# Kernel tuning notes

Hardware: AMD Instinct MI355X
Metric: run time of the kernel (lower is better)

## Reference

```python
import jax, jax.numpy as jnp
import numpy as np
from functools import partial

B, N, C = 16, 10647, 80   # batch, total anchors (YOLOv3@416), num classes
K = 2048                  # max candidates kept per image before NMS
SCORE_THR = 0.5
IOU_THR = 0.5


def setup_inputs() -> dict:
    key = jax.random.key(0)
    # [B, N, 4+1+C]: xywh (normalized), objectness, class probs
    y_pred = jax.random.uniform(key, (B, N, 5 + C), dtype=jnp.float32)
    return {"y_pred": y_pred}


def _xywh_to_corners(b):
    x, y, w, h = b[..., 0], b[..., 1], b[..., 2], b[..., 3]
    return jnp.stack([x - w / 2, y - h / 2, x + w / 2, y + h / 2], axis=-1)


def _pairwise_iou(boxes):  # boxes [K,4] corners -> [K,K]
    x1, y1, x2, y2 = boxes[:, 0], boxes[:, 1], boxes[:, 2], boxes[:, 3]
    area = jnp.maximum(x2 - x1, 0.0) * jnp.maximum(y2 - y1, 0.0)
    ix1 = jnp.maximum(x1[:, None], x1[None, :])
    iy1 = jnp.maximum(y1[:, None], y1[None, :])
    ix2 = jnp.minimum(x2[:, None], x2[None, :])
    iy2 = jnp.minimum(y2[:, None], y2[None, :])
    inter = jnp.maximum(ix2 - ix1, 0.0) * jnp.maximum(iy2 - iy1, 0.0)
    union = area[:, None] + area[None, :] - inter
    return inter / jnp.maximum(union, 1e-9)


def _greedy_nms_keep(boxes, valid):  # boxes [K,4] sorted by score desc, valid [K] bool
    iou = _pairwise_iou(boxes)
    idxs = jnp.arange(K)

    def body(i, keep):
        suppress = keep[i] & (idxs > i) & (iou[i] > IOU_THR)
        return keep & ~suppress

    return jax.lax.fori_loop(0, K, body, valid)


def reference(y_pred):
    boxes_xywh = y_pred[..., :4]           # [B,N,4]
    obj = y_pred[..., 4]                   # [B,N]
    cls_probs = y_pred[..., 5:]            # [B,N,C]
    scores = obj * jnp.max(cls_probs, axis=-1)  # [B,N]

    # top-K candidates per image (sorted by score desc)
    scores_k, idx = jax.lax.top_k(scores, K)             # [B,K]
    boxes_k = jnp.take_along_axis(boxes_xywh, idx[:, :, None], axis=1)  # [B,K,4]
    corners = _xywh_to_corners(boxes_k)                  # [B,K,4]

    valid = scores_k > SCORE_THR                          # [B,K]
    # NMS keep mask is a non-differentiable selection
    keep = jax.vmap(_greedy_nms_keep)(
        jax.lax.stop_gradient(corners), valid)            # [B,K] bool
    keep_f = keep.astype(scores_k.dtype)

    out_boxes = corners * keep_f[:, :, None]
    out_scores = scores_k * keep_f
    return jnp.concatenate([out_boxes, out_scores[:, :, None]], axis=-1)  # [B,K,5]
```

## Files before the change

kernel.cpp:

```cpp
#include <hip/hip_runtime.h>

#define BATCH 16
#define NROW  10647
#define ROWF  85
#define NCLS  80
#define KTOP  2048
#define MPAD  16384
#define SCORE_THR 0.5f
#define IOU_THR   0.5f

typedef unsigned long long u64;
typedef unsigned int u32;

__device__ __forceinline__ u32 enc_f32(float f) {
    u32 u = __float_as_uint(f);
    return (u & 0x80000000u) ? ~u : (u | 0x80000000u);
}
__device__ __forceinline__ float dec_f32(u32 e) {
    u32 u = (e & 0x80000000u) ? (e & 0x7FFFFFFFu) : ~e;
    return __uint_as_float(u);
}
__device__ __forceinline__ float bcast(float v, int ii) {
    return __uint_as_float(__builtin_amdgcn_readlane(__float_as_uint(v), ii));
}
__device__ __forceinline__ u64 rl64(u64 v, int l) {
    u32 lo = __builtin_amdgcn_readlane((u32)(v & 0xFFFFFFFFull), l);
    u32 hi = __builtin_amdgcn_readlane((u32)(v >> 32), l);
    return ((u64)hi << 32) | (u64)lo;
}
__device__ __forceinline__ void gload_lds16(const void* g, void* lds) {
    __builtin_amdgcn_global_load_lds(
        (const __attribute__((address_space(1))) void*)g,
        (__attribute__((address_space(3))) void*)lds, 16, 0, 0);
}
__device__ __forceinline__ void bar_lds() {
    asm volatile("s_waitcnt lgkmcnt(0)" ::: "memory");
    __builtin_amdgcn_s_barrier();
    __builtin_amdgcn_sched_barrier(0);
}

template<int J>
__device__ __forceinline__ void reg_pass(u64 v[8], int tid, int k) {
    #pragma unroll
    for (int r = 0; r < 8; ++r) {
        if (!(r & J)) {
            bool desc = (((tid * 8 + r) & k) == 0);
            u64 a = v[r], b = v[r | J];
            u64 mx = a > b ? a : b, mn = a > b ? b : a;
            v[r]     = desc ? mx : mn;
            v[r | J] = desc ? mn : mx;
        }
    }
}

__device__ __forceinline__ void shfl_pass(u64 v[8], int tid, int k, int d) {
    const bool upper = (tid & d) == 0;
    const bool desc = (((tid * 8) & k) == 0);
    const bool keepmax = (desc == upper);
    #pragma unroll
    for (int r = 0; r < 8; ++r) {
        u64 pv = __shfl_xor(v[r], d);
        u64 mx = v[r] > pv ? v[r] : pv, mn = v[r] > pv ? pv : v[r];
        v[r] = keepmax ? mx : mn;
    }
}

__device__ __forceinline__ void lds_pass(u64 v[8], int tid, u64* sm, int k, int d) {
    __syncthreads();
    #pragma unroll
    for (int r = 0; r < 8; ++r) sm[r * 256 + tid] = v[r];
    __syncthreads();
    const bool upper = (tid & d) == 0;
    const bool desc = (((tid * 8) & k) == 0);
    const bool keepmax = (desc == upper);
    const int pt = tid ^ d;
    #pragma unroll
    for (int r = 0; r < 8; ++r) {
        u64 pv = sm[r * 256 + pt];
        u64 mx = v[r] > pv ? v[r] : pv, mn = v[r] > pv ? pv : v[r];
        v[r] = keepmax ? mx : mn;
    }
}

__device__ __forceinline__ void sort2048_desc(u64 v[8], int tid, u64* sm) {
    reg_pass<1>(v, tid, 2);
    reg_pass<2>(v, tid, 4); reg_pass<1>(v, tid, 4);
    for (int k = 8; k <= 2048; k <<= 1) {
        for (int j = k >> 1; j >= 8; j >>= 1) {
            int d = j >> 3;
            if (d <= 32) shfl_pass(v, tid, k, d);
            else         lds_pass(v, tid, sm, k, d);
        }
        reg_pass<4>(v, tid, k); reg_pass<2>(v, tid, k); reg_pass<1>(v, tid, k);
    }
}

__device__ __forceinline__ void cleanup2048_desc(u64 v[8], int tid, u64* sm) {
    lds_pass(v, tid, sm, 4096, 128);
    lds_pass(v, tid, sm, 4096, 64);
    for (int d = 32; d >= 1; d >>= 1) shfl_pass(v, tid, 4096, d);
    reg_pass<4>(v, tid, 4096); reg_pass<2>(v, tid, 4096); reg_pass<1>(v, tid, 4096);
}

__global__ void score_kernel(const float* __restrict__ yp, u64* __restrict__ keys) {
    __shared__ float tile[128 * ROWF];
    const int tileIdx = blockIdx.x;
    const int b = blockIdx.y;
    const int tid = threadIdx.x;
    const int batch_lim = NROW * ROWF;
    const int tile_base = tileIdx * 128 * ROWF;

    if (tile_base < batch_lim) {
        const float* src = yp + (long long)b * batch_lim + tile_base;
        int lim_e = batch_lim - tile_base;
        if (lim_e > 128 * ROWF) lim_e = 128 * ROWF;
        const int head = (4 - ((3 * b) & 3)) & 3;
        if (lim_e >= 8) {
            const int nv = (lim_e - head) >> 2;
            for (int e = tid; e < head; e += 256) tile[e] = src[e];
            const float4* s4 = (const float4*)(src + head);
            for (int q = tid; q < nv; q += 256) {
                float4 v = s4[q];
                int o = head + q * 4;
                tile[o] = v.x; tile[o + 1] = v.y; tile[o + 2] = v.z; tile[o + 3] = v.w;
            }
            for (int e = head + nv * 4 + tid; e < lim_e; e += 256) tile[e] = src[e];
        } else {
            for (int e = tid; e < lim_e; e += 256) tile[e] = src[e];
        }
    }
    __syncthreads();

    {
        const int row = tid >> 1;
        const int half = tid & 1;
        int gr = tileIdx * 128 + row;
        const float* r = &tile[row * ROWF];
        float m = r[5 + half * 40];
        #pragma unroll
        for (int c = 1; c < 40; ++c) m = fmaxf(m, r[5 + half * 40 + c]);
        float mo = __uint_as_float(__shfl_xor(__float_as_uint(m), 1));
        if (half == 0 && gr < NROW) {
            float s = r[4] * fmaxf(m, mo);
            keys[(long long)b * MPAD + gr] =
                ((u64)enc_f32(s) << 32) | (u64)(0xFFFFFFFFu - (u32)gr);
        } else if (half == 0) {
            keys[(long long)b * MPAD + gr] = 0ULL;
        }
    }
}

__global__ void chunk_sort_kernel(u64* __restrict__ keys) {
    __shared__ u64 sm[2048];
    const int b = blockIdx.y, c = blockIdx.x, tid = threadIdx.x;
    u64* base = keys + (long long)b * MPAD + c * 2048;
    u64 v[8];
    #pragma unroll
    for (int r = 0; r < 8; ++r) v[r] = base[tid * 8 + r];
    sort2048_desc(v, tid, sm);
    #pragma unroll
    for (int r = 0; r < 8; ++r) base[tid * 8 + r] = v[r];
}

__global__ void merge_r1_kernel(const u64* __restrict__ keysA, u64* __restrict__ keysB) {
    __shared__ u64 sm[2048];
    const int b = blockIdx.y, c = blockIdx.x, tid = threadIdx.x;
    const u64* a = keysA + (long long)b * MPAD + c * 4096;
    u64 v[8];
    #pragma unroll
    for (int r = 0; r < 8; ++r) {
        int e = tid * 8 + r;
        u64 va = a[e], vb = a[4095 - e];
        v[r] = va > vb ? va : vb;
    }
    cleanup2048_desc(v, tid, sm);
    u64* d = keysB + (long long)b * MPAD + c * 2048;
    #pragma unroll
    for (int r = 0; r < 8; ++r) d[tid * 8 + r] = v[r];
}

__global__ void merge_r23_gather_kernel(const u64* __restrict__ keysB,
                                        const float* __restrict__ yp,
                                        float* __restrict__ sx1, float* __restrict__ sy1,
                                        float* __restrict__ sx2, float* __restrict__ sy2,
                                        float* __restrict__ sar, float* __restrict__ ssc) {
    __shared__ u64 sm[2048];
    const int b = blockIdx.x, tid = threadIdx.x;
    const u64* a = keysB + (long long)b * MPAD;
    u64 v[8];
    #pragma unroll
    for (int r = 0; r < 8; ++r) {
        int e = tid * 8 + r;
        u64 va = a[e], vb = a[2048 + 2047 - e];
        v[r] = va > vb ? va : vb;
    }
    cleanup2048_desc(v, tid, sm);
    #pragma unroll
    for (int r = 0; r < 8; ++r) {
        int e = tid * 8 + r;
        u64 vb = a[4096 + 2047 - e];
        v[r] = v[r] > vb ? v[r] : vb;
    }
    cleanup2048_desc(v, tid, sm);

    #pragma unroll
    for (int r = 0; r < 8; ++r) {
        u64 key = v[r];
        float s = dec_f32((u32)(key >> 32));
        u32 idx = 0xFFFFFFFFu - (u32)(key & 0xFFFFFFFFu);
        const float* rp = yp + (long long)b * NROW * ROWF + (long long)idx * ROWF;
        float x = rp[0], y = rp[1], w = rp[2], h = rp[3];
        float hx = w * 0.5f, hy = h * 0.5f;
        float a1 = x - hx, b1 = y - hy, a2 = x + hx, b2 = y + hy;
        int o = b * KTOP + tid * 8 + r;
        sx1[o] = a1; sy1[o] = b1; sx2[o] = a2; sy2[o] = b2;
        sar[o] = fmaxf(a2 - a1, 0.f) * fmaxf(b2 - b1, 0.f);
        ssc[o] = s;
    }
}

__global__ void mask_kernel(const float* __restrict__ sx1, const float* __restrict__ sy1,
                            const float* __restrict__ sx2, const float* __restrict__ sy2,
                            const float* __restrict__ sar, u64* __restrict__ mask,
                            u64* __restrict__ diag) {
    const int b = blockIdx.y;
    const int t = blockIdx.x * 4 + (threadIdx.x >> 6);
    const int lane = threadIdx.x & 63;

    int rb = (int)((65.0f - sqrtf(4225.0f - 8.0f * (float)t)) * 0.5f);
    while (rb * (65 - rb) / 2 > t) --rb;
    while ((rb + 1) * (64 - rb) / 2 <= t) ++rb;
    const int cb = rb + t - rb * (65 - rb) / 2;

    const int oi = b * KTOP + rb * 64 + lane;
    const int oj = b * KTOP + cb * 64 + lane;
    const float rx1 = sx1[oi], ry1 = sy1[oi], rx2 = sx2[oi], ry2 = sy2[oi], ra = sar[oi];
    const float cx1 = sx1[oj], cy1 = sy1[oj], cx2 = sx2[oj], cy2 = sy2[oj], ca = sar[oj];
    const bool dg = (rb == cb);

    u64 myword = 0ULL;
    for (int ii = 0; ii < 64; ++ii) {
        float ax1 = bcast(rx1, ii), ay1 = bcast(ry1, ii);
        float ax2 = bcast(rx2, ii), ay2 = bcast(ry2, ii);
        float aa  = bcast(ra,  ii);
        float ix1 = fmaxf(ax1, cx1);
        float iy1 = fmaxf(ay1, cy1);
        float ix2 = fminf(ax2, cx2);
        float iy2 = fminf(ay2, cy2);
        float inter = fmaxf(ix2 - ix1, 0.f) * fmaxf(iy2 - iy1, 0.f);
        float uni = aa + ca - inter;
        float iou = inter / fmaxf(uni, 1e-9f);
        bool cond = (iou > IOU_THR) && (!dg || (lane > ii));
        u64 bal = __ballot(cond);
        if (lane == ii) myword = bal;
    }
    mask[(long long)(b * KTOP + rb * 64 + lane) * 32 + cb] = myword;
    if (dg) diag[(long long)b * 2048 + rb * 64 + lane] = myword;
}

__global__ void nms_out_kernel(const float* __restrict__ sx1, const float* __restrict__ sy1,
                               const float* __restrict__ sx2, const float* __restrict__ sy2,
                               const float* __restrict__ ssc,
                               const u64* __restrict__ mask,
                               const u64* __restrict__ diag, float* __restrict__ out) {
    __shared__ u64 slots[4][2048];
    __shared__ u64 pend[8][32];
    __shared__ u64 curs;
    __shared__ u64 sbits64[32];
    __shared__ u64 keepw[32];
    const int b = blockIdx.x;
    const int tid = threadIdx.x;
    const int lane = tid & 63;
    const int wave = tid >> 6;
    const u64* mb = mask + (long long)(b * KTOP) * 32;
    const char* mbc = (const char*)mb;
    const u64* dg = diag + (long long)b * 2048;

    auto issue_block = [&](int B) {
        const char* src = mbc + (size_t)B * 16384;
        char* dst = (char*)&slots[B & 3][0];
        #pragma unroll
        for (int i = 0; i < 16; ++i)
            gload_lds16(src + i * 1024 + lane * 16, dst + i * 1024);
    };

    {
        const float* sp = ssc + b * KTOP + tid * 8;
        float4 sa = *(const float4*)(sp);
        float4 sb = *(const float4*)(sp + 4);
        unsigned bits =
            (unsigned)(sa.x > SCORE_THR)       | ((unsigned)(sa.y > SCORE_THR) << 1) |
            ((unsigned)(sa.z > SCORE_THR) << 2) | ((unsigned)(sa.w > SCORE_THR) << 3) |
            ((unsigned)(sb.x > SCORE_THR) << 4) | ((unsigned)(sb.y > SCORE_THR) << 5) |
            ((unsigned)(sb.z > SCORE_THR) << 6) | ((unsigned)(sb.w > SCORE_THR) << 7);
        ((unsigned char*)sbits64)[tid] = (unsigned char)bits;
    }
    u64 dia = 0ULL;
    if (wave == 0) dia = dg[lane];
    if (wave >= 1) issue_block(wave - 1);
    __syncthreads();

    u64 myw = 0ULL;
    if (wave == 0 && lane < 32) myw = sbits64[lane];

    #pragma unroll 1
    for (int w = 0; w < 32; ++w) {
        const u64* blk = &slots[w & 3][0];

        if (wave == 0) {
            u64 dia_next = 0ULL;
            if (w < 31) dia_next = dg[(w + 1) * 64 + lane];
            u64 cur = rl64(myw, w);
            #pragma unroll
            for (int p = 0; p < 4; ++p) {
                u64 dd[16];
                #pragma unroll
                for (int i = 0; i < 16; ++i) dd[i] = rl64(dia, p * 16 + i);
                #pragma unroll
                for (int i = 0; i < 16; ++i) {
                    u64 m = ((cur >> (p * 16 + i)) & 1ULL) ? dd[i] : 0ULL;
                    cur &= ~m;
                }
            }
            if (lane == 0) curs = cur;
            dia = dia_next;
        } else {
            const int rr = wave - 1;
            if ((w % 3) == rr && w + 3 < 32) issue_block(w + 3);
            if (((w + 1) % 3) == rr)
                asm volatile("s_waitcnt vmcnt(0)" ::: "memory");
        }
        bar_lds();

        {
            u64 curv = curs;
            const int col = tid & 31;
            const int rg  = tid >> 5;
            const u64* rp = blk + (size_t)rg * 256 + col;
            u32 bits8 = (u32)(curv >> (rg * 8)) & 0xFFu;
            u64 acc = 0ULL;
            #pragma unroll
            for (int i = 0; i < 8; ++i) {
                u64 t = rp[(size_t)i * 32];
                acc |= ((bits8 >> i) & 1u) ? t : 0ULL;
            }
            pend[rg][col] = acc;
        }
        bar_lds();

        if (wave == 0 && lane < 32) {
            u64 cur = curs;
            u64 s = ((pend[0][lane] | pend[1][lane]) | (pend[2][lane] | pend[3][lane]))
                  | ((pend[4][lane] | pend[5][lane]) | (pend[6][lane] | pend[7][lane]));
            if (lane == w) myw = cur;
            else if (lane > w) myw &= ~s;
        }
    }

    if (wave == 0 && lane < 32) keepw[lane] = myw;
    __syncthreads();

    for (int t = tid; t < KTOP; t += 256) {
        int o = b * KTOP + t;
        float f = ((keepw[t >> 6] >> (t & 63)) & 1ULL) ? 1.0f : 0.0f;
        float* op = out + (long long)o * 5;
        op[0] = sx1[o] * f;
        op[1] = sy1[o] * f;
        op[2] = sx2[o] * f;
        op[3] = sy2[o] * f;
        op[4] = ssc[o] * f;
    }
}

extern "C" void kernel_launch(void* const* d_in, const int* in_sizes, int n_in,
                              void* d_out, int out_size, void* d_ws, size_t ws_size,
                              hipStream_t stream) {
    const float* yp = (const float*)d_in[0];
    float* out = (float*)d_out;
    char* ws = (char*)d_ws;

    const size_t KEYS_BYTES = (size_t)BATCH * MPAD * sizeof(u64);
    const size_t MASK_BYTES = (size_t)BATCH * KTOP * 32 * sizeof(u64);
    const size_t SOA_BYTES  = (size_t)6 * BATCH * KTOP * sizeof(float);
    u64* keysA = (u64*)ws;
    u64* keysB = (u64*)(ws + KEYS_BYTES);
    u64* mask  = (u64*)ws;
    float* soa = (float*)(ws + MASK_BYTES);
    u64* diag  = (u64*)(ws + MASK_BYTES + SOA_BYTES);
    const int SA = BATCH * KTOP;
    float* sx1 = soa + 0 * SA;
    float* sy1 = soa + 1 * SA;
    float* sx2 = soa + 2 * SA;
    float* sy2 = soa + 3 * SA;
    float* sar = soa + 4 * SA;
    float* ssc = soa + 5 * SA;

    score_kernel<<<dim3(96, BATCH), 256, 0, stream>>>(yp, keysA);
    chunk_sort_kernel<<<dim3(6, BATCH), 256, 0, stream>>>(keysA);
    merge_r1_kernel<<<dim3(3, BATCH), 256, 0, stream>>>(keysA, keysB);
    merge_r23_gather_kernel<<<BATCH, 256, 0, stream>>>(keysB, yp,
                                                       sx1, sy1, sx2, sy2, sar, ssc);
    mask_kernel<<<dim3(132, BATCH), 256, 0, stream>>>(sx1, sy1, sx2, sy2, sar,
                                                      mask, diag);
    nms_out_kernel<<<BATCH, 256, 0, stream>>>(sx1, sy1, sx2, sy2, ssc,
                                              mask, diag, out);
}
```

Measured before the change: 161.8 us.

## Pack NMS suppression mask as upper-triangular rows to halve mask traffic

The mask kernel now writes only the upper-triangular column blocks of each 64-row block into a packed per-image layout, with row stride padded to an even word count. The NMS kernel streams only those words into LDS per row block, so the serial NMS stage loads about half as much mask data. In exchange, addressing becomes variable-stride and the per-block load loop is no longer fully unrolled. Columns left of the diagonal are clamped to a valid offset and rely on existing masking to ignore them.

```diff
diff --git a/kernel.cpp b/kernel.cpp
--- a/kernel.cpp
+++ b/kernel.cpp
@@ -8,6 +8,7 @@
 #define MPAD  16384
 #define SCORE_THR 0.5f
 #define IOU_THR   0.5f
+#define PKWORDS 34816
 
 typedef unsigned long long u64;
 typedef unsigned int u32;
@@ -28,6 +29,8 @@
     u32 hi = __builtin_amdgcn_readlane((u32)(v >> 32), l);
     return ((u64)hi << 32) | (u64)lo;
 }
+__device__ __forceinline__ int wpad(int B) { return 32 - B + (B & 1); }
+__device__ __forceinline__ int soff(int B) { return 32 * B - (B * (B - 1)) / 2 + (B >> 1); }
 __device__ __forceinline__ void gload_lds16(const void* g, void* lds) {
     __builtin_amdgcn_global_load_lds(
         (const __attribute__((address_space(1))) void*)g,
@@ -221,7 +224,7 @@
 
 __global__ void mask_kernel(const float* __restrict__ sx1, const float* __restrict__ sy1,
                             const float* __restrict__ sx2, const float* __restrict__ sy2,
-                            const float* __restrict__ sar, u64* __restrict__ mask,
+                            const float* __restrict__ sar, u64* __restrict__ packed,
                             u64* __restrict__ diag) {
     const int b = blockIdx.y;
     const int t = blockIdx.x * 4 + (threadIdx.x >> 6);
@@ -254,14 +257,15 @@
         u64 bal = __ballot(cond);
         if (lane == ii) myword = bal;
     }
-    mask[(long long)(b * KTOP + rb * 64 + lane) * 32 + cb] = myword;
+    const int wB = wpad(rb);
+    packed[(long long)b * PKWORDS + 64 * soff(rb) + lane * wB + (cb - rb)] = myword;
     if (dg) diag[(long long)b * 2048 + rb * 64 + lane] = myword;
 }
 
 __global__ void nms_out_kernel(const float* __restrict__ sx1, const float* __restrict__ sy1,
                                const float* __restrict__ sx2, const float* __restrict__ sy2,
                                const float* __restrict__ ssc,
-                               const u64* __restrict__ mask,
+                               const u64* __restrict__ packed,
                                const u64* __restrict__ diag, float* __restrict__ out) {
     __shared__ u64 slots[4][2048];
     __shared__ u64 pend[8][32];
@@ -272,15 +276,14 @@
     const int tid = threadIdx.x;
     const int lane = tid & 63;
     const int wave = tid >> 6;
-    const u64* mb = mask + (long long)(b * KTOP) * 32;
-    const char* mbc = (const char*)mb;
+    const u64* pk = packed + (long long)b * PKWORDS;
     const u64* dg = diag + (long long)b * 2048;
 
     auto issue_block = [&](int B) {
-        const char* src = mbc + (size_t)B * 16384;
+        const char* src = (const char*)(pk + (size_t)64 * soff(B));
         char* dst = (char*)&slots[B & 3][0];
-        #pragma unroll
-        for (int i = 0; i < 16; ++i)
+        const int nch = wpad(B) >> 1;
+        for (int i = 0; i < nch; ++i)
             gload_lds16(src + i * 1024 + lane * 16, dst + i * 1024);
     };
 
@@ -336,12 +339,14 @@
             u64 curv = curs;
             const int col = tid & 31;
             const int rg  = tid >> 5;
-            const u64* rp = blk + (size_t)rg * 256 + col;
+            const int wB = wpad(w);
+            int jo = col - w; if (jo < 0) jo = 0;
+            const u64* rp = blk + (size_t)(rg * 8) * wB + jo;
             u32 bits8 = (u32)(curv >> (rg * 8)) & 0xFFu;
             u64 acc = 0ULL;
             #pragma unroll
             for (int i = 0; i < 8; ++i) {
-                u64 t = rp[(size_t)i * 32];
+                u64 t = rp[(size_t)i * wB];
                 acc |= ((bits8 >> i) & 1u) ? t : 0ULL;
             }
             pend[rg][col] = acc;
@@ -382,11 +387,11 @@
     const size_t KEYS_BYTES = (size_t)BATCH * MPAD * sizeof(u64);
     const size_t MASK_BYTES = (size_t)BATCH * KTOP * 32 * sizeof(u64);
     const size_t SOA_BYTES  = (size_t)6 * BATCH * KTOP * sizeof(float);
-    u64* keysA = (u64*)ws;
-    u64* keysB = (u64*)(ws + KEYS_BYTES);
-    u64* mask  = (u64*)ws;
-    float* soa = (float*)(ws + MASK_BYTES);
-    u64* diag  = (u64*)(ws + MASK_BYTES + SOA_BYTES);
+    u64* keysA  = (u64*)ws;
+    u64* keysB  = (u64*)(ws + KEYS_BYTES);
+    u64* packed = (u64*)ws;
+    float* soa  = (float*)(ws + MASK_BYTES);
+    u64* diag   = (u64*)(ws + MASK_BYTES + SOA_BYTES);
     const int SA = BATCH * KTOP;
     float* sx1 = soa + 0 * SA;
     float* sy1 = soa + 1 * SA;
@@ -401,7 +406,7 @@
     merge_r23_gather_kernel<<<BATCH, 256, 0, stream>>>(keysB, yp,
                                                        sx1, sy1, sx2, sy2, sar, ssc);
     mask_kernel<<<dim3(132, BATCH), 256, 0, stream>>>(sx1, sy1, sx2, sy2, sar,
-                                                      mask, diag);
+                                                      packed, diag);
     nms_out_kernel<<<BATCH, 256, 0, stream>>>(sx1, sy1, sx2, sy2, ssc,
-                                              mask, diag, out);
-}
+                                              packed, diag, out);
+}
```

Result: no change. 158.7 us (-1.9%).
